# Optimization experiments

Measured on AMD Instinct MI355X. Metric: run time of the kernel, lower is better.

Reference implementation:

```python
import jax, jax.numpy as jnp
import numpy as np

L, D, H, N, R = 4, 256, 512, 16, 8  # layers, d_model, hidden=2*d_model, state_dim, dt_rank
OUT_LEN, IN_DIM = 96, 32
EPS = 1e-5


def _layernorm(v, g, b):
    m = jnp.mean(v, axis=-1, keepdims=True)
    var = jnp.mean((v - m) ** 2, axis=-1, keepdims=True)
    return (v - m) / jnp.sqrt(var + EPS) * g + b


def _pos_encoding(T, d):
    pos = jnp.arange(T, dtype=jnp.float32)[:, None]
    div = jnp.exp(jnp.arange(0, d, 2, dtype=jnp.float32) * (-np.log(10000.0) / d))
    pe = jnp.zeros((T, d), dtype=jnp.float32)
    pe = pe.at[:, 0::2].set(jnp.sin(pos * div))
    pe = pe.at[:, 1::2].set(jnp.cos(pos * div))
    return pe


def setup_inputs() -> dict:
    key = jax.random.key(0)
    ks = jax.random.split(key, 20)
    inp = {
        "x": jax.random.normal(ks[0], (8, 1024, IN_DIM), dtype=jnp.float32),
        "emb_w": jax.random.normal(ks[1], (D, IN_DIM), dtype=jnp.float32) * 0.1,
        "emb_b": jnp.zeros((D,), dtype=jnp.float32),
        "norm_g": jnp.ones((L, D), dtype=jnp.float32),
        "norm_b": jnp.zeros((L, D), dtype=jnp.float32),
        "in_w": jax.random.normal(ks[2], (L, H, D), dtype=jnp.float32) * (1.0 / np.sqrt(D)),
        "conv_w": jax.random.normal(ks[3], (L, H, 1, 3), dtype=jnp.float32) * 0.5,
        "A_p": jax.random.normal(ks[4], (L, H, N), dtype=jnp.float32) * 0.01,
        "D_p": jnp.ones((L, H), dtype=jnp.float32),
        "dt1_w": jax.random.normal(ks[5], (L, R, H), dtype=jnp.float32) * (1.0 / np.sqrt(H)),
        "dt1_b": jnp.zeros((L, R), dtype=jnp.float32),
        "dt2_w": jax.random.normal(ks[6], (L, H, R), dtype=jnp.float32) * (1.0 / np.sqrt(R)),
        "dt2_b": jnp.zeros((L, H), dtype=jnp.float32),
        "out_w": jax.random.normal(ks[7], (L, D, H), dtype=jnp.float32) * (1.0 / np.sqrt(H)),
        "final_g": jnp.ones((D,), dtype=jnp.float32),
        "final_b": jnp.zeros((D,), dtype=jnp.float32),
        "head1_w": jax.random.normal(ks[8], (D, D), dtype=jnp.float32) * (1.0 / np.sqrt(D)),
        "head1_b": jnp.zeros((D,), dtype=jnp.float32),
        "head2_w": jax.random.normal(ks[9], (OUT_LEN, D), dtype=jnp.float32) * (1.0 / np.sqrt(D)),
        "head2_b": jnp.zeros((OUT_LEN,), dtype=jnp.float32),
    }
    return inp


def _mamba_block(h, g, b, in_w, conv_w, A_p, D_p, dt1_w, dt1_b, dt2_w, dt2_b, out_w):
    res = h
    v = _layernorm(h, g, b)            # [B,T,D]
    v = jnp.einsum('btd,hd->bth', v, in_w)  # [B,T,H]
    # depthwise conv1d, kernel 3, padding 1, groups=H
    vc = jnp.transpose(v, (0, 2, 1))   # [B,H,T]
    vc = jax.lax.conv_general_dilated(vc, conv_w, window_strides=(1,),
                                      padding=[(1, 1)], feature_group_count=H,
                                      dimension_numbers=('NCH', 'OIH', 'NCH'))
    v = jnp.transpose(jax.nn.silu(vc), (0, 2, 1))  # [B,T,H]
    dt = jax.nn.relu(jnp.einsum('bth,rh->btr', v, dt1_w) + dt1_b)
    dt = jnp.einsum('btr,hr->bth', dt, dt2_w) + dt2_b
    dt = jax.nn.softplus(dt)           # [B,T,H]
    A = -jnp.exp(A_p)                  # [H,N]
    safe_A = jnp.where(jnp.abs(A) < 1e-5, jnp.ones_like(A), A)

    B_sz = v.shape[0]
    state0 = jnp.zeros((B_sz, H, N), dtype=v.dtype)

    def step(state, inp):
        x_t, dt_t = inp  # [B,H] each
        dA = A * dt_t[..., None]            # [B,H,N]
        discA = jnp.exp(dA)
        discB = (discA - 1.0) / safe_A * dt_t[..., None]
        state = discA * state + discB * x_t[..., None]
        y = jnp.einsum('bhn,hn->bh', state, A_p) + D_p * x_t
        return state, y

    xs = (jnp.transpose(v, (1, 0, 2)), jnp.transpose(dt, (1, 0, 2)))  # [T,B,H]
    _, ys = jax.lax.scan(step, state0, xs)
    y = jnp.transpose(ys, (1, 0, 2))   # [B,T,H]
    return res + jnp.einsum('bth,dh->btd', y, out_w)


def reference(x, emb_w, emb_b, norm_g, norm_b, in_w, conv_w, A_p, D_p,
              dt1_w, dt1_b, dt2_w, dt2_b, out_w, final_g, final_b,
              head1_w, head1_b, head2_w, head2_b):
    h = jnp.einsum('bti,di->btd', x, emb_w) + emb_b  # [B,T,D]
    h = h + _pos_encoding(h.shape[1], D)[None]
    for l in range(L):
        h = _mamba_block(h, norm_g[l], norm_b[l], in_w[l], conv_w[l], A_p[l],
                         D_p[l], dt1_w[l], dt1_b[l], dt2_w[l], dt2_b[l], out_w[l])
    h = _layernorm(h, final_g, final_b)
    h = h[:, -1, :]                    # last token [B,D]
    h = jax.nn.silu(h @ head1_w.T + head1_b)
    return h @ head2_w.T + head2_b     # [B, OUT_LEN]
```

## Files before the change

### kernel.cpp

```cpp
#include <hip/hip_runtime.h>
#include <hip/hip_bf16.h>
#include <math.h>

#define BB 8
#define TT 1024
#define DD 256
#define HH 512
#define NN 16
#define RR 8
#define OUT_LEN 96
#define IN_DIM 32
#define MM (BB*TT)

#define SC 16
#define CC (TT/SC)

typedef unsigned short u16;
typedef unsigned int u32;
typedef __attribute__((ext_vector_type(8))) short short8;
typedef __attribute__((ext_vector_type(8))) unsigned short u16x8;
typedef __attribute__((ext_vector_type(4))) float float4v;

__device__ __forceinline__ u16 f2bf(float f) {
    __hip_bfloat16 h = __float2bfloat16(f);
    return *(u16*)&h;
}
__device__ __forceinline__ float bf2f(u16 u) {
    u32 v = ((u32)u) << 16;
    return *(float*)&v;
}

#define GLD_LDS16(src, dst) __builtin_amdgcn_global_load_lds( \
    (const __attribute__((address_space(1))) void*)(src),     \
    (__attribute__((address_space(3))) void*)(dst), 16, 0, 0)

#define SBAR()   asm volatile("s_barrier" ::: "memory")
#define VMCNT0() asm volatile("s_waitcnt vmcnt(0)" ::: "memory")
#define VMCNT6() asm volatile("s_waitcnt vmcnt(6)" ::: "memory")
#define VMCNT9() asm volatile("s_waitcnt vmcnt(9)" ::: "memory")

__global__ __launch_bounds__(256) void embed_ln_cvt_kernel(
    const float* __restrict__ x, const float* __restrict__ emb_w,
    const float* __restrict__ emb_b,
    const float* __restrict__ g, const float* __restrict__ b,
    float* __restrict__ h, u16* __restrict__ lnout,
    const float* __restrict__ w_in, u16* __restrict__ wbf_in,
    const float* __restrict__ w_out, u16* __restrict__ wbf_out, int nw)
{
    int bid = blockIdx.x;
    if (bid >= MM) {
        int i = (bid - MM) * 256 + threadIdx.x;
        if (i < nw) wbf_in[i] = f2bf(w_in[i]);
        else        wbf_out[i - nw] = f2bf(w_out[i - nw]);
        return;
    }

    int bt = bid;
    int d  = threadIdx.x;
    int t  = bt & (TT - 1);

    __shared__ float xs[IN_DIM];
    __shared__ float red[4], red2[4];
    if (threadIdx.x < IN_DIM) xs[threadIdx.x] = x[bt * IN_DIM + threadIdx.x];
    __syncthreads();

    const float* w = emb_w + d * IN_DIM;
    float acc = emb_b[d];
#pragma unroll
    for (int i = 0; i < IN_DIM; i++) acc = fmaf(xs[i], w[i], acc);

    int i2 = d & ~1;
    float div = __expf(-(float)i2 * 0.0359778918f);
    float arg = (float)t * div;
    float pe = (d & 1) ? __cosf(arg) : __sinf(arg);
    float val = acc + pe;
    h[bt * DD + d] = val;

    float s = val;
#pragma unroll
    for (int o = 32; o > 0; o >>= 1) s += __shfl_down(s, o);
    int lane = d & 63, wave = d >> 6;
    if (lane == 0) red[wave] = s;
    __syncthreads();
    float mean = (red[0] + red[1] + red[2] + red[3]) * (1.0f / DD);

    float c = val - mean;
    float s2 = c * c;
#pragma unroll
    for (int o = 32; o > 0; o >>= 1) s2 += __shfl_down(s2, o);
    if (lane == 0) red2[wave] = s2;
    __syncthreads();
    float var = (red2[0] + red2[1] + red2[2] + red2[3]) * (1.0f / DD);

    lnout[bt * DD + d] = f2bf(c * rsqrtf(var + 1e-5f) * g[d] + b[d]);
}

template<int BM, int BN, int OUT_BF16>
__global__ __launch_bounds__(256) void gemm_bf16(
    const u16* __restrict__ A, const u16* __restrict__ B,
    void* __restrict__ Cv, int M, int N, int K, int addC)
{
    constexpr int BK = 64;
    constexpr int MT = BM / 32;
    constexpr int NT = BN / 32;
    static_assert(BM == 128 && BN == 64, "vmcnt count assumes 6 loads/thread");

    __shared__ __align__(16) u16 Al[2][8][BM][8];
    __shared__ __align__(16) u16 Bl[2][8][BN][8];

    const int tid = threadIdx.x;
    const int bm = blockIdx.y * BM;
    const int bn = blockIdx.x * BN;
    const int wid = tid >> 6, lane = tid & 63;
    const int wm = wid >> 1, wn = wid & 1;
    const int lq = lane >> 4, lm = lane & 15;

    float4v acc[MT][NT];
#pragma unroll
    for (int i = 0; i < MT; i++)
#pragma unroll
        for (int j = 0; j < NT; j++) acc[i][j] = (float4v){0.f, 0.f, 0.f, 0.f};

#pragma unroll
    for (int it = 0; it < (8 * BM) / 256; it++) {
        int c = it * 256 + tid;
        int q = c / BM, row = c % BM;
        GLD_LDS16(A + (size_t)(bm + row) * K + q * 8, &Al[0][q][row][0]);
    }
#pragma unroll
    for (int it = 0; it < (8 * BN) / 256; it++) {
        int c = it * 256 + tid;
        int q = c / BN, row = c % BN;
        GLD_LDS16(B + (size_t)(bn + row) * K + q * 8, &Bl[0][q][row][0]);
    }

    const int nt = K / BK;
    int cur = 0;
    for (int i = 0; i < nt; i++) {
        if (i + 1 < nt) {
            int nxt = cur ^ 1;
            int k1 = (i + 1) * BK;
#pragma unroll
            for (int it = 0; it < (8 * BM) / 256; it++) {
                int c = it * 256 + tid;
                int q = c / BM, row = c % BM;
                GLD_LDS16(A + (size_t)(bm + row) * K + k1 + q * 8, &Al[nxt][q][row][0]);
            }
#pragma unroll
            for (int it = 0; it < (8 * BN) / 256; it++) {
                int c = it * 256 + tid;
                int q = c / BN, row = c % BN;
                GLD_LDS16(B + (size_t)(bn + row) * K + k1 + q * 8, &Bl[nxt][q][row][0]);
            }
            VMCNT6();
        } else {
            VMCNT0();
        }
        SBAR();

        short8 af[2][MT], bf[2][NT];
#pragma unroll
        for (int kk = 0; kk < 2; kk++) {
#pragma unroll
            for (int mt = 0; mt < MT; mt++)
                af[kk][mt] = *(const short8*)&Al[cur][kk * 4 + lq][wm * (BM / 2) + mt * 16 + lm][0];
#pragma unroll
            for (int nt2 = 0; nt2 < NT; nt2++)
                bf[kk][nt2] = *(const short8*)&Bl[cur][kk * 4 + lq][wn * (BN / 2) + nt2 * 16 + lm][0];
        }

#pragma unroll
        for (int kk = 0; kk < 2; kk++)
#pragma unroll
            for (int mt = 0; mt < MT; mt++)
#pragma unroll
                for (int nt2 = 0; nt2 < NT; nt2++)
                    acc[mt][nt2] = __builtin_amdgcn_mfma_f32_16x16x32_bf16(
                        af[kk][mt], bf[kk][nt2], acc[mt][nt2], 0, 0, 0);
        SBAR();
        cur ^= 1;
    }

#pragma unroll
    for (int mt = 0; mt < MT; mt++)
#pragma unroll
        for (int nt2 = 0; nt2 < NT; nt2++) {
            int row0 = bm + wm * (BM / 2) + mt * 16 + lq * 4;
            int col  = bn + wn * (BN / 2) + nt2 * 16 + lm;
#pragma unroll
            for (int r = 0; r < 4; r++) {
                float vv = acc[mt][nt2][r];
                if (OUT_BF16) {
                    ((u16*)Cv)[(size_t)(row0 + r) * N + col] = f2bf(vv);
                } else {
                    float* cp = (float*)Cv + (size_t)(row0 + r) * N + col;
                    if (addC) vv += *cp;
                    *cp = vv;
                }
            }
        }
}

__global__ __launch_bounds__(256) void gemm2_ln(
    const u16* __restrict__ A, const u16* __restrict__ B,
    float* __restrict__ h,
    const float* __restrict__ g, const float* __restrict__ bb,
    u16* __restrict__ lnout, int doLN)
{
    constexpr int BM = 32;
    __shared__ __align__(16) u16 Al[2][8][BM][8];
    __shared__ __align__(16) u16 Bl[2][8][256][8];
    __shared__ float rs[2][BM], qs[2][BM];

    const int tid = threadIdx.x;
    const int bm = blockIdx.x * BM;
    const int wid = tid >> 6, lane = tid & 63;
    const int wm = wid >> 1, wn = wid & 1;
    const int lq = lane >> 4, lm = lane & 15;

    float4v acc[8];
#pragma unroll
    for (int j = 0; j < 8; j++) acc[j] = (float4v){0.f, 0.f, 0.f, 0.f};

    {
        int q = tid >> 5, row = tid & 31;
        GLD_LDS16(A + (size_t)(bm + row) * 512 + q * 8, &Al[0][q][row][0]);
    }
#pragma unroll
    for (int it = 0; it < 8; it++) {
        int c = it * 256 + tid;
        int q = c >> 8, row = c & 255;
        GLD_LDS16(B + (size_t)row * 512 + q * 8, &Bl[0][q][row][0]);
    }

    int cur = 0;
    for (int i = 0; i < 8; i++) {
        if (i + 1 < 8) {
            int nxt = cur ^ 1;
            int k1 = (i + 1) * 64;
            {
                int q = tid >> 5, row = tid & 31;
                GLD_LDS16(A + (size_t)(bm + row) * 512 + k1 + q * 8, &Al[nxt][q][row][0]);
            }
#pragma unroll
            for (int it = 0; it < 8; it++) {
                int c = it * 256 + tid;
                int q = c >> 8, row = c & 255;
                GLD_LDS16(B + (size_t)row * 512 + k1 + q * 8, &Bl[nxt][q][row][0]);
            }
            VMCNT9();
        } else {
            VMCNT0();
        }
        SBAR();

        short8 af[2], bf[2][8];
#pragma unroll
        for (int kk = 0; kk < 2; kk++) {
            af[kk] = *(const short8*)&Al[cur][kk * 4 + lq][wm * 16 + lm][0];
#pragma unroll
            for (int nt = 0; nt < 8; nt++)
                bf[kk][nt] = *(const short8*)&Bl[cur][kk * 4 + lq][wn * 128 + nt * 16 + lm][0];
        }
#pragma unroll
        for (int kk = 0; kk < 2; kk++)
#pragma unroll
            for (int nt = 0; nt < 8; nt++)
                acc[nt] = __builtin_amdgcn_mfma_f32_16x16x32_bf16(
                    af[kk], bf[kk][nt], acc[nt], 0, 0, 0);
        SBAR();
        cur ^= 1;
    }

    float val[4][8];
    float s1[4] = {0.f, 0.f, 0.f, 0.f}, s2[4] = {0.f, 0.f, 0.f, 0.f};
#pragma unroll
    for (int r = 0; r < 4; r++) {
        int row = bm + wm * 16 + lq * 4 + r;
#pragma unroll
        for (int nt = 0; nt < 8; nt++) {
            int col = wn * 128 + nt * 16 + lm;
            float v = acc[nt][r] + h[(size_t)row * DD + col];
            val[r][nt] = v;
            s1[r] += v;
            s2[r] = fmaf(v, v, s2[r]);
            h[(size_t)row * DD + col] = v;
        }
    }
#pragma unroll
    for (int r = 0; r < 4; r++) {
#pragma unroll
        for (int o = 1; o < 16; o <<= 1) {
            s1[r] += __shfl_xor(s1[r], o);
            s2[r] += __shfl_xor(s2[r], o);
        }
    }
    if (lm == 0) {
#pragma unroll
        for (int r = 0; r < 4; r++) {
            rs[wn][wm * 16 + lq * 4 + r] = s1[r];
            qs[wn][wm * 16 + lq * 4 + r] = s2[r];
        }
    }
    __syncthreads();

    if (doLN) {
#pragma unroll
        for (int r = 0; r < 4; r++) {
            int i = wm * 16 + lq * 4 + r;
            int row = bm + i;
            float mean = (rs[0][i] + rs[1][i]) * (1.0f / DD);
            float var  = (qs[0][i] + qs[1][i]) * (1.0f / DD) - mean * mean;
            float rstd = rsqrtf(var + 1e-5f);
#pragma unroll
            for (int nt = 0; nt < 8; nt++) {
                int col = wn * 128 + nt * 16 + lm;
                lnout[(size_t)row * DD + col] =
                    f2bf((val[r][nt] - mean) * rstd * g[col] + bb[col]);
            }
        }
    }
}

__device__ __forceinline__ float softplus_f(float s) {
    return (s > 20.0f) ? s : __logf(1.0f + __expf(s));
}

__global__ __launch_bounds__(512, 4) void conv_scan1(
    const u16* __restrict__ vbf, const float* __restrict__ cwg,
    const float* __restrict__ w1g, const float* __restrict__ b1g,
    const float* __restrict__ dt2_w, const float* __restrict__ dt2_b,
    const float* __restrict__ A_p,
    u16* __restrict__ vsb, float* __restrict__ dtr,
    u16* __restrict__ Lst, float* __restrict__ sdt)
{
    const int c = blockIdx.x;
    const int b = blockIdx.y;
    const int tid = threadIdx.x;
    const int wave = tid >> 6, lane = tid & 63;
    const int h0 = lane * 8;

    __shared__ float w1s[RR * 2 * 256];
    __shared__ u16   a_lds[SC][HH];
    __shared__ float ds[SC * RR];

#pragma unroll
    for (int i = 0; i < 2; i++) {
        int rci = wave + i * 8;
        int r = rci >> 1, jc = rci & 1;
        float4 wv = *(const float4*)(w1g + r * HH + lane * 8 + jc * 4);
        *(float4*)&w1s[rci * 256 + lane * 4] = wv;
    }
    __syncthreads();

    const float* wp = cwg + h0 * 3;
#pragma unroll
    for (int i = 0; i < 2; i++) {
        int tr = wave + i * 8;
        int t  = c * SC + tr;
        size_t m = (size_t)b * TT + t;

        const u16* vrow = vbf + m * HH + h0;
        u16x8 x0 = *(const u16x8*)vrow;
        u16x8 xm = (t > 0)      ? *(const u16x8*)(vrow - HH) : (u16x8)(0);
        u16x8 xp = (t < TT - 1) ? *(const u16x8*)(vrow + HH) : (u16x8)(0);

        float a[8];
        u16x8 o;
#pragma unroll
        for (int j = 0; j < 8; j++) {
            float s = wp[j * 3] * bf2f(xm[j]);
            s = fmaf(wp[j * 3 + 1], bf2f(x0[j]), s);
            s = fmaf(wp[j * 3 + 2], bf2f(xp[j]), s);
            s = s / (1.0f + __expf(-s));
            a[j] = s;
            o[j] = f2bf(s);
        }
        *(u16x8*)(vsb + m * HH + h0) = o;
        *(u16x8*)&a_lds[tr][h0]      = o;

        float acc[RR];
#pragma unroll
        for (int r = 0; r < RR; r++) {
            float4 wlo = *(const float4*)&w1s[(r * 2 + 0) * 256 + lane * 4];
            float4 whi = *(const float4*)&w1s[(r * 2 + 1) * 256 + lane * 4];
            float s = a[0] * wlo.x;
            s = fmaf(a[1], wlo.y, s);
            s = fmaf(a[2], wlo.z, s);
            s = fmaf(a[3], wlo.w, s);
            s = fmaf(a[4], whi.x, s);
            s = fmaf(a[5], whi.y, s);
            s = fmaf(a[6], whi.z, s);
            s = fmaf(a[7], whi.w, s);
            acc[r] = s;
        }
#pragma unroll
        for (int r = 0; r < RR; r++) {
#pragma unroll
            for (int o2 = 1; o2 < 64; o2 <<= 1) acc[r] += __shfl_xor(acc[r], o2);
        }
        if (lane == 0) {
#pragma unroll
            for (int r = 0; r < RR; r++) acc[r] = fmaxf(acc[r] + b1g[r], 0.0f);
            *(float4*)(dtr + m * RR)     = make_float4(acc[0], acc[1], acc[2], acc[3]);
            *(float4*)(dtr + m * RR + 4) = make_float4(acc[4], acc[5], acc[6], acc[7]);
#pragma unroll
            for (int r = 0; r < RR; r++) ds[tr * RR + r] = acc[r];
        }
    }
    __syncthreads();

    const int h = tid;
    float A2[NN], invA[NN], st[NN];
    const float* ap = A_p + h * NN;
#pragma unroll
    for (int n = 0; n < NN; n++) {
        float av = -__expf(ap[n]);
        A2[n] = av * 1.44269504f;
        invA[n] = 1.0f / av;
        st[n] = 0.0f;
    }
    float w2[RR];
#pragma unroll
    for (int r = 0; r < RR; r++) w2[r] = dt2_w[h * RR + r];
    float b2 = dt2_b[h];

    float xv = bf2f(a_lds[0][h]);
    float s_dt = 0.0f;
#pragma unroll 2
    for (int t = 0; t < SC; t++) {
        float xn = (t + 1 < SC) ? bf2f(a_lds[t + 1][h]) : 0.0f;
        float s = b2;
#pragma unroll
        for (int r = 0; r < RR; r++) s = fmaf(ds[t * RR + r], w2[r], s);
        float dt = softplus_f(s);
        s_dt += dt;
        float dtx = dt * xv;
#pragma unroll
        for (int n = 0; n < NN; n++) {
            float e = __builtin_amdgcn_exp2f(A2[n] * dt);
            float u = invA[n] * dtx;
            st[n] = fmaf(e, st[n] + u, -u);
        }
        xv = xn;
    }

    size_t base = (((size_t)c * BB + b) * HH + h) * NN;
    u16x8 lo, hi;
#pragma unroll
    for (int n = 0; n < 8; n++) { lo[n] = f2bf(st[n]); hi[n] = f2bf(st[n + 8]); }
    *(u16x8*)(Lst + base)     = lo;
    *(u16x8*)(Lst + base + 8) = hi;
    sdt[((size_t)c * BB + b) * HH + h] = s_dt;
}

__global__ __launch_bounds__(256) void scan_carry_par(
    const float* __restrict__ A_p, const float* __restrict__ sdt,
    u16* __restrict__ Lst)
{
    int gw   = (blockIdx.x << 2) | (threadIdx.x >> 6);
    int lane = threadIdx.x & 63;
    int b = gw >> 9;
    int h = gw & 511;

    size_t sidx = ((size_t)lane * BB + b) * HH + h;
    float sd = sdt[sidx];
    const float* ap = A_p + h * NN;
    u16x8 Llo = *(const u16x8*)(Lst + sidx * NN);
    u16x8 Lhi = *(const u16x8*)(Lst + sidx * NN + 8);
    u16x8 Elo, Ehi;
#pragma unroll
    for (int n = 0; n < NN; n++) {
        float An = -__expf(ap[n]);
        float p  = __expf(An * sd);
        float lv = bf2f((n < 8) ? Llo[n] : Lhi[n - 8]);
#pragma unroll
        for (int d2 = 1; d2 < 64; d2 <<= 1) {
            float pp = __shfl_up(p, d2);
            float pl = __shfl_up(lv, d2);
            if (lane >= d2) { lv = fmaf(pl, p, lv); p = pp * p; }
        }
        float E = __shfl_up(lv, 1);
        if (lane == 0) E = 0.0f;
        if (n < 8) Elo[n] = f2bf(E); else Ehi[n - 8] = f2bf(E);
    }
    *(u16x8*)(Lst + sidx * NN)     = Elo;
    *(u16x8*)(Lst + sidx * NN + 8) = Ehi;
}

__global__ __launch_bounds__(256, 4) void scan_pass2(
    const u16* __restrict__ vs,
    const float* __restrict__ dtr,
    const float* __restrict__ dt2_w,
    const float* __restrict__ dt2_b,
    const float* __restrict__ A_p, const float* __restrict__ D_p,
    const u16* __restrict__ carry,
    u16* __restrict__ y)
{
    int h = blockIdx.x * 256 + threadIdx.x;
    int c = blockIdx.y;
    int b = blockIdx.z;

    __shared__ float ds[SC * RR];
    {
        const float* drow = dtr + ((size_t)b * TT + (size_t)c * SC) * RR;
        if (threadIdx.x < SC * RR) ds[threadIdx.x] = drow[threadIdx.x];
    }

    float A2[NN], invA[NN], Ap[NN], st[NN];
    const float* app = A_p + h * NN;
    size_t cbase = (((size_t)c * BB + b) * HH + h) * NN;
    {
        u16x8 lo = *(const u16x8*)(carry + cbase);
        u16x8 hi = *(const u16x8*)(carry + cbase + 8);
#pragma unroll
        for (int n = 0; n < 8; n++) { st[n] = bf2f(lo[n]); st[n + 8] = bf2f(hi[n]); }
    }
#pragma unroll
    for (int n = 0; n < NN; n++) {
        float apv = app[n];
        Ap[n] = apv;
        float a = -__expf(apv);
        A2[n] = a * 1.44269504f;
        invA[n] = 1.0f / a;
    }
    float w2[RR];
#pragma unroll
    for (int r = 0; r < RR; r++) w2[r] = dt2_w[h * RR + r];
    float b2 = dt2_b[h];
    float Dp = D_p[h];

    const u16* vbase = vs + ((size_t)b * TT + (size_t)c * SC) * HH + h;
    u16*       ybase = y  + ((size_t)b * TT + (size_t)c * SC) * HH + h;
    float xv = bf2f(vbase[0]);
    __syncthreads();

#pragma unroll 2
    for (int t = 0; t < SC; t++) {
        float xn = (t + 1 < SC) ? bf2f(vbase[(size_t)(t + 1) * HH]) : 0.0f;
        float s = b2;
#pragma unroll
        for (int r = 0; r < RR; r++) s = fmaf(ds[t * RR + r], w2[r], s);
        float dt = softplus_f(s);
        float dtx = dt * xv;
        float acc = Dp * xv;
#pragma unroll
        for (int n = 0; n < NN; n++) {
            float e = __builtin_amdgcn_exp2f(A2[n] * dt);
            float u = invA[n] * dtx;
            st[n] = fmaf(e, st[n] + u, -u);
            acc = fmaf(st[n], Ap[n], acc);
        }
        ybase[(size_t)t * HH] = f2bf(acc);
        xv = xn;
    }
}

__global__ __launch_bounds__(256) void head_kernel(
    const float* __restrict__ h,
    const float* __restrict__ fg, const float* __restrict__ fb,
    const float* __restrict__ w1, const float* __restrict__ b1,
    const float* __restrict__ w2, const float* __restrict__ b2,
    float* __restrict__ out)
{
    int b = blockIdx.x;
    int d = threadIdx.x;
    __shared__ float hn[DD], s1[DD];
    __shared__ float red[4];

    float v = h[((size_t)b * TT + (TT - 1)) * DD + d];

    float s = v;
#pragma unroll
    for (int o = 32; o > 0; o >>= 1) s += __shfl_down(s, o);
    int lane = d & 63, wave = d >> 6;
    if (lane == 0) red[wave] = s;
    __syncthreads();
    float mean = (red[0] + red[1] + red[2] + red[3]) * (1.0f / DD);
    __syncthreads();

    float c = v - mean;
    float s2 = c * c;
#pragma unroll
    for (int o = 32; o > 0; o >>= 1) s2 += __shfl_down(s2, o);
    if (lane == 0) red[wave] = s2;
    __syncthreads();
    float var = (red[0] + red[1] + red[2] + red[3]) * (1.0f / DD);

    hn[d] = c * rsqrtf(var + 1e-5f) * fg[d] + fb[d];
    __syncthreads();

    float a1 = b1[d];
    const float* w1r = w1 + d * DD;
#pragma unroll 8
    for (int k = 0; k < DD; k++) a1 = fmaf(hn[k], w1r[k], a1);
    s1[d] = a1 / (1.0f + __expf(-a1));
    __syncthreads();

    if (d < OUT_LEN) {
        float a2 = b2[d];
        const float* w2r = w2 + d * DD;
#pragma unroll 8
        for (int k = 0; k < DD; k++) a2 = fmaf(s1[k], w2r[k], a2);
        out[b * OUT_LEN + d] = a2;
    }
}

extern "C" void kernel_launch(void* const* d_in, const int* in_sizes, int n_in,
                              void* d_out, int out_size, void* d_ws, size_t ws_size,
                              hipStream_t stream)
{
    (void)in_sizes; (void)n_in; (void)out_size; (void)ws_size;

    const float* x       = (const float*)d_in[0];
    const float* emb_w   = (const float*)d_in[1];
    const float* emb_b   = (const float*)d_in[2];
    const float* norm_g  = (const float*)d_in[3];
    const float* norm_b  = (const float*)d_in[4];
    const float* in_w    = (const float*)d_in[5];
    const float* conv_w  = (const float*)d_in[6];
    const float* A_p     = (const float*)d_in[7];
    const float* D_p     = (const float*)d_in[8];
    const float* dt1_w   = (const float*)d_in[9];
    const float* dt1_b   = (const float*)d_in[10];
    const float* dt2_w   = (const float*)d_in[11];
    const float* dt2_b   = (const float*)d_in[12];
    const float* out_w   = (const float*)d_in[13];
    const float* final_g = (const float*)d_in[14];
    const float* final_b = (const float*)d_in[15];
    const float* head1_w = (const float*)d_in[16];
    const float* head1_b = (const float*)d_in[17];
    const float* head2_w = (const float*)d_in[18];
    const float* head2_b = (const float*)d_in[19];
    float* outp = (float*)d_out;

    char* ws = (char*)d_ws;
    float* h     = (float*)ws;                ws += (size_t)MM * DD * 4;
    u16*   vbf   = (u16*)ws;                  ws += (size_t)MM * HH * 2;
    u16*   vsb   = (u16*)ws;                  ws += (size_t)MM * HH * 2;
    u16*   ybf   = (u16*)ws;                  ws += (size_t)MM * HH * 2;
    u16*   lnbuf = (u16*)ws;                  ws += (size_t)MM * DD * 2;
    float* dtr   = (float*)ws;                ws += (size_t)MM * RR * 4;
    u16*   Lst   = (u16*)ws;                  ws += (size_t)CC * BB * HH * NN * 2;
    float* sdt   = (float*)ws;                ws += (size_t)CC * BB * HH * 4;
    u16*   wbf_in  = (u16*)ws;                ws += (size_t)4 * HH * DD * 2;
    u16*   wbf_out = (u16*)ws;                ws += (size_t)4 * DD * HH * 2;

    const int NW = 4 * HH * DD;
    embed_ln_cvt_kernel<<<MM + (2 * NW) / 256, 256, 0, stream>>>(
        x, emb_w, emb_b, norm_g, norm_b, h, lnbuf,
        in_w, wbf_in, out_w, wbf_out, NW);

    for (int l = 0; l < 4; l++) {
        gemm_bf16<128, 64, 1><<<dim3(HH / 64, MM / 128), 256, 0, stream>>>(
            lnbuf, wbf_in + (size_t)l * HH * DD, vbf, MM, HH, DD, 0);

        conv_scan1<<<dim3(CC, BB), 512, 0, stream>>>(
            vbf, conv_w + (size_t)l * HH * 3,
            dt1_w + (size_t)l * RR * HH, dt1_b + l * RR,
            dt2_w + (size_t)l * HH * RR, dt2_b + l * HH,
            A_p + (size_t)l * HH * NN,
            vsb, dtr, Lst, sdt);

        scan_carry_par<<<(BB * HH) / 4, 256, 0, stream>>>(
            A_p + (size_t)l * HH * NN, sdt, Lst);

        scan_pass2<<<dim3(HH / 256, CC, BB), 256, 0, stream>>>(
            vsb, dtr, dt2_w + (size_t)l * HH * RR, dt2_b + l * HH,
            A_p + (size_t)l * HH * NN, D_p + l * HH, Lst, ybf);

        const float* g_next = (l < 3) ? (norm_g + (l + 1) * DD) : final_g;
        const float* b_next = (l < 3) ? (norm_b + (l + 1) * DD) : final_b;
        gemm2_ln<<<MM / 32, 256, 0, stream>>>(
            ybf, wbf_out + (size_t)l * DD * HH, h, g_next, b_next,
            lnbuf, (l < 3) ? 1 : 0);
    }

    head_kernel<<<BB, 256, 0, stream>>>(h, final_g, final_b,
                                        head1_w, head1_b, head2_w, head2_b, outp);
}
```

Baseline: 485.7 us.

## Fuse scan pass2 into out-projection GEMM with LayerNorm epilogue

Merges the second scan pass and the out-projection GEMM+LayerNorm into one kernel. Each 512-thread block scans 32 timesteps (two chunks) for all 512 hidden channels, writes y into an XOR-swizzled LDS tile, and then runs the MFMA GEMM against the out_w tile straight from LDS. This removes the bf16 y buffer round trip through global memory and one kernel launch per layer. In exchange there are fewer blocks in flight (large LDS, 512 threads), each thread runs a serial scan over 32 steps, and the GEMM N-split across waves becomes finer.

```diff
diff --git a/kernel.cpp b/kernel.cpp
--- a/kernel.cpp
+++ b/kernel.cpp
@@ -36,8 +36,8 @@
 
 #define SBAR()   asm volatile("s_barrier" ::: "memory")
 #define VMCNT0() asm volatile("s_waitcnt vmcnt(0)" ::: "memory")
+#define VMCNT4() asm volatile("s_waitcnt vmcnt(4)" ::: "memory")
 #define VMCNT6() asm volatile("s_waitcnt vmcnt(6)" ::: "memory")
-#define VMCNT9() asm volatile("s_waitcnt vmcnt(9)" ::: "memory")
 
 __global__ __launch_bounds__(256) void embed_ln_cvt_kernel(
     const float* __restrict__ x, const float* __restrict__ emb_w,
@@ -201,127 +201,6 @@
         }
 }
 
-__global__ __launch_bounds__(256) void gemm2_ln(
-    const u16* __restrict__ A, const u16* __restrict__ B,
-    float* __restrict__ h,
-    const float* __restrict__ g, const float* __restrict__ bb,
-    u16* __restrict__ lnout, int doLN)
-{
-    constexpr int BM = 32;
-    __shared__ __align__(16) u16 Al[2][8][BM][8];
-    __shared__ __align__(16) u16 Bl[2][8][256][8];
-    __shared__ float rs[2][BM], qs[2][BM];
-
-    const int tid = threadIdx.x;
-    const int bm = blockIdx.x * BM;
-    const int wid = tid >> 6, lane = tid & 63;
-    const int wm = wid >> 1, wn = wid & 1;
-    const int lq = lane >> 4, lm = lane & 15;
-
-    float4v acc[8];
-#pragma unroll
-    for (int j = 0; j < 8; j++) acc[j] = (float4v){0.f, 0.f, 0.f, 0.f};
-
-    {
-        int q = tid >> 5, row = tid & 31;
-        GLD_LDS16(A + (size_t)(bm + row) * 512 + q * 8, &Al[0][q][row][0]);
-    }
-#pragma unroll
-    for (int it = 0; it < 8; it++) {
-        int c = it * 256 + tid;
-        int q = c >> 8, row = c & 255;
-        GLD_LDS16(B + (size_t)row * 512 + q * 8, &Bl[0][q][row][0]);
-    }
-
-    int cur = 0;
-    for (int i = 0; i < 8; i++) {
-        if (i + 1 < 8) {
-            int nxt = cur ^ 1;
-            int k1 = (i + 1) * 64;
-            {
-                int q = tid >> 5, row = tid & 31;
-                GLD_LDS16(A + (size_t)(bm + row) * 512 + k1 + q * 8, &Al[nxt][q][row][0]);
-            }
-#pragma unroll
-            for (int it = 0; it < 8; it++) {
-                int c = it * 256 + tid;
-                int q = c >> 8, row = c & 255;
-                GLD_LDS16(B + (size_t)row * 512 + k1 + q * 8, &Bl[nxt][q][row][0]);
-            }
-            VMCNT9();
-        } else {
-            VMCNT0();
-        }
-        SBAR();
-
-        short8 af[2], bf[2][8];
-#pragma unroll
-        for (int kk = 0; kk < 2; kk++) {
-            af[kk] = *(const short8*)&Al[cur][kk * 4 + lq][wm * 16 + lm][0];
-#pragma unroll
-            for (int nt = 0; nt < 8; nt++)
-                bf[kk][nt] = *(const short8*)&Bl[cur][kk * 4 + lq][wn * 128 + nt * 16 + lm][0];
-        }
-#pragma unroll
-        for (int kk = 0; kk < 2; kk++)
-#pragma unroll
-            for (int nt = 0; nt < 8; nt++)
-                acc[nt] = __builtin_amdgcn_mfma_f32_16x16x32_bf16(
-                    af[kk], bf[kk][nt], acc[nt], 0, 0, 0);
-        SBAR();
-        cur ^= 1;
-    }
-
-    float val[4][8];
-    float s1[4] = {0.f, 0.f, 0.f, 0.f}, s2[4] = {0.f, 0.f, 0.f, 0.f};
-#pragma unroll
-    for (int r = 0; r < 4; r++) {
-        int row = bm + wm * 16 + lq * 4 + r;
-#pragma unroll
-        for (int nt = 0; nt < 8; nt++) {
-            int col = wn * 128 + nt * 16 + lm;
-            float v = acc[nt][r] + h[(size_t)row * DD + col];
-            val[r][nt] = v;
-            s1[r] += v;
-            s2[r] = fmaf(v, v, s2[r]);
-            h[(size_t)row * DD + col] = v;
-        }
-    }
-#pragma unroll
-    for (int r = 0; r < 4; r++) {
-#pragma unroll
-        for (int o = 1; o < 16; o <<= 1) {
-            s1[r] += __shfl_xor(s1[r], o);
-            s2[r] += __shfl_xor(s2[r], o);
-        }
-    }
-    if (lm == 0) {
-#pragma unroll
-        for (int r = 0; r < 4; r++) {
-            rs[wn][wm * 16 + lq * 4 + r] = s1[r];
-            qs[wn][wm * 16 + lq * 4 + r] = s2[r];
-        }
-    }
-    __syncthreads();
-
-    if (doLN) {
-#pragma unroll
-        for (int r = 0; r < 4; r++) {
-            int i = wm * 16 + lq * 4 + r;
-            int row = bm + i;
-            float mean = (rs[0][i] + rs[1][i]) * (1.0f / DD);
-            float var  = (qs[0][i] + qs[1][i]) * (1.0f / DD) - mean * mean;
-            float rstd = rsqrtf(var + 1e-5f);
-#pragma unroll
-            for (int nt = 0; nt < 8; nt++) {
-                int col = wn * 128 + nt * 16 + lm;
-                lnout[(size_t)row * DD + col] =
-                    f2bf((val[r][nt] - mean) * rstd * g[col] + bb[col]);
-            }
-        }
-    }
-}
-
 __device__ __forceinline__ float softplus_f(float s) {
     return (s > 20.0f) ? s : __logf(1.0f + __expf(s));
 }
@@ -488,71 +367,186 @@
     *(u16x8*)(Lst + sidx * NN + 8) = Ehi;
 }
 
-__global__ __launch_bounds__(256, 4) void scan_pass2(
-    const u16* __restrict__ vs,
-    const float* __restrict__ dtr,
-    const float* __restrict__ dt2_w,
-    const float* __restrict__ dt2_b,
+__global__ __launch_bounds__(512) void scan2_gemm2_ln(
+    const u16* __restrict__ vsb, const float* __restrict__ dtr,
+    const float* __restrict__ dt2_w, const float* __restrict__ dt2_b,
     const float* __restrict__ A_p, const float* __restrict__ D_p,
     const u16* __restrict__ carry,
-    u16* __restrict__ y)
+    const u16* __restrict__ B,
+    float* __restrict__ h,
+    const float* __restrict__ g, const float* __restrict__ bb,
+    u16* __restrict__ lnout, int doLN)
 {
-    int h = blockIdx.x * 256 + threadIdx.x;
-    int c = blockIdx.y;
-    int b = blockIdx.z;
-
-    __shared__ float ds[SC * RR];
-    {
-        const float* drow = dtr + ((size_t)b * TT + (size_t)c * SC) * RR;
-        if (threadIdx.x < SC * RR) ds[threadIdx.x] = drow[threadIdx.x];
-    }
-
-    float A2[NN], invA[NN], Ap[NN], st[NN];
-    const float* app = A_p + h * NN;
-    size_t cbase = (((size_t)c * BB + b) * HH + h) * NN;
-    {
-        u16x8 lo = *(const u16x8*)(carry + cbase);
-        u16x8 hi = *(const u16x8*)(carry + cbase + 8);
-#pragma unroll
-        for (int n = 0; n < 8; n++) { st[n] = bf2f(lo[n]); st[n + 8] = bf2f(hi[n]); }
-    }
+    const int bid = blockIdx.x;
+    const int b   = bid >> 5;
+    const int tb  = bid & 31;
+    const int t0  = tb * 32;
+    const int c0  = tb * 2;
+    const int bm  = bid * 32;
+
+    const int tid = threadIdx.x;
+    const int wid = tid >> 6;
+    const int lane = tid & 63;
+    const int lq = lane >> 4, lm = lane & 15;
+    const int wm = wid >> 2;
+    const int wn = wid & 3;
+
+    __shared__ __align__(16) u16 Yl[32 * 512];
+    __shared__ __align__(16) u16 Bl[2][8][256][8];
+    __shared__ float ds[32 * RR];
+    __shared__ float rs[4][32], qs[4][32];
+
+#pragma unroll
+    for (int it = 0; it < 4; it++) {
+        int cth = it * 512 + tid;
+        int q = cth >> 8, row = cth & 255;
+        GLD_LDS16(B + (size_t)row * 512 + q * 8, &Bl[0][q][row][0]);
+    }
+
+    if (tid < 256) {
+        int tr = tid >> 3, r = tid & 7;
+        ds[tid] = dtr[((size_t)b * TT + t0 + tr) * RR + r];
+    }
+
+    const int hh = tid;
+    float A2[NN], invA[NN], Ap[NN], w2[RR];
+    const float* ap = A_p + hh * NN;
 #pragma unroll
     for (int n = 0; n < NN; n++) {
-        float apv = app[n];
-        Ap[n] = apv;
+        float apv = ap[n]; Ap[n] = apv;
         float a = -__expf(apv);
-        A2[n] = a * 1.44269504f;
-        invA[n] = 1.0f / a;
-    }
-    float w2[RR];
-#pragma unroll
-    for (int r = 0; r < RR; r++) w2[r] = dt2_w[h * RR + r];
-    float b2 = dt2_b[h];
-    float Dp = D_p[h];
-
-    const u16* vbase = vs + ((size_t)b * TT + (size_t)c * SC) * HH + h;
-    u16*       ybase = y  + ((size_t)b * TT + (size_t)c * SC) * HH + h;
-    float xv = bf2f(vbase[0]);
-    __syncthreads();
-
+        A2[n] = a * 1.44269504f; invA[n] = 1.0f / a;
+    }
+#pragma unroll
+    for (int r = 0; r < RR; r++) w2[r] = dt2_w[hh * RR + r];
+    float b2 = dt2_b[hh];
+    float Dp = D_p[hh];
+    __syncthreads();
+
+#pragma unroll
+    for (int cc = 0; cc < 2; cc++) {
+        int cg = c0 + cc;
+        float st[NN];
+        size_t cbase = (((size_t)cg * BB + b) * HH + hh) * NN;
+        u16x8 clo = *(const u16x8*)(carry + cbase);
+        u16x8 chi = *(const u16x8*)(carry + cbase + 8);
+#pragma unroll
+        for (int n = 0; n < 8; n++) { st[n] = bf2f(clo[n]); st[n + 8] = bf2f(chi[n]); }
+
+        const u16* vbase = vsb + ((size_t)b * TT + (size_t)cg * SC) * HH + hh;
+        float xv = bf2f(vbase[0]);
 #pragma unroll 2
-    for (int t = 0; t < SC; t++) {
-        float xn = (t + 1 < SC) ? bf2f(vbase[(size_t)(t + 1) * HH]) : 0.0f;
-        float s = b2;
-#pragma unroll
-        for (int r = 0; r < RR; r++) s = fmaf(ds[t * RR + r], w2[r], s);
-        float dt = softplus_f(s);
-        float dtx = dt * xv;
-        float acc = Dp * xv;
-#pragma unroll
-        for (int n = 0; n < NN; n++) {
-            float e = __builtin_amdgcn_exp2f(A2[n] * dt);
-            float u = invA[n] * dtx;
-            st[n] = fmaf(e, st[n] + u, -u);
-            acc = fmaf(st[n], Ap[n], acc);
-        }
-        ybase[(size_t)t * HH] = f2bf(acc);
-        xv = xn;
+        for (int t = 0; t < SC; t++) {
+            float xn = (t + 1 < SC) ? bf2f(vbase[(size_t)(t + 1) * HH]) : 0.0f;
+            int tr = cc * SC + t;
+            float s = b2;
+#pragma unroll
+            for (int r = 0; r < RR; r++) s = fmaf(ds[tr * RR + r], w2[r], s);
+            float dt = softplus_f(s);
+            float dtx = dt * xv;
+            float acc = Dp * xv;
+#pragma unroll
+            for (int n = 0; n < NN; n++) {
+                float e = __builtin_amdgcn_exp2f(A2[n] * dt);
+                float u = invA[n] * dtx;
+                st[n] = fmaf(e, st[n] + u, -u);
+                acc = fmaf(st[n], Ap[n], acc);
+            }
+            Yl[tr * 512 + (hh ^ ((tr & 7) << 3))] = f2bf(acc);
+            xv = xn;
+        }
+    }
+    __syncthreads();
+
+    float4v acc4[4];
+#pragma unroll
+    for (int j = 0; j < 4; j++) acc4[j] = (float4v){0.f, 0.f, 0.f, 0.f};
+
+    int cur = 0;
+    for (int i = 0; i < 8; i++) {
+        if (i + 1 < 8) {
+            int nxt = cur ^ 1;
+            int k1 = (i + 1) * 64;
+#pragma unroll
+            for (int it = 0; it < 4; it++) {
+                int cth = it * 512 + tid;
+                int q = cth >> 8, row = cth & 255;
+                GLD_LDS16(B + (size_t)row * 512 + k1 + q * 8, &Bl[nxt][q][row][0]);
+            }
+            VMCNT4();
+        } else {
+            VMCNT0();
+        }
+        SBAR();
+
+        int k0 = i * 64;
+        short8 af[2], bf[2][4];
+#pragma unroll
+        for (int kk = 0; kk < 2; kk++) {
+            int row = wm * 16 + lm;
+            int kg  = (k0 >> 3) + kk * 4 + lq;
+            af[kk] = *(const short8*)&Yl[row * 512 + ((kg ^ (row & 7)) << 3)];
+#pragma unroll
+            for (int nt = 0; nt < 4; nt++)
+                bf[kk][nt] = *(const short8*)&Bl[cur][kk * 4 + lq][wn * 64 + nt * 16 + lm][0];
+        }
+#pragma unroll
+        for (int kk = 0; kk < 2; kk++)
+#pragma unroll
+            for (int nt = 0; nt < 4; nt++)
+                acc4[nt] = __builtin_amdgcn_mfma_f32_16x16x32_bf16(
+                    af[kk], bf[kk][nt], acc4[nt], 0, 0, 0);
+        SBAR();
+        cur ^= 1;
+    }
+
+    float val[4][4];
+    float s1[4] = {0.f, 0.f, 0.f, 0.f}, s2[4] = {0.f, 0.f, 0.f, 0.f};
+#pragma unroll
+    for (int r = 0; r < 4; r++) {
+        int row = bm + wm * 16 + lq * 4 + r;
+#pragma unroll
+        for (int nt = 0; nt < 4; nt++) {
+            int col = wn * 64 + nt * 16 + lm;
+            float v = acc4[nt][r] + h[(size_t)row * DD + col];
+            val[r][nt] = v;
+            s1[r] += v;
+            s2[r] = fmaf(v, v, s2[r]);
+            h[(size_t)row * DD + col] = v;
+        }
+    }
+#pragma unroll
+    for (int r = 0; r < 4; r++) {
+#pragma unroll
+        for (int o = 1; o < 16; o <<= 1) {
+            s1[r] += __shfl_xor(s1[r], o);
+            s2[r] += __shfl_xor(s2[r], o);
+        }
+    }
+    if (lm == 0) {
+#pragma unroll
+        for (int r = 0; r < 4; r++) {
+            rs[wn][wm * 16 + lq * 4 + r] = s1[r];
+            qs[wn][wm * 16 + lq * 4 + r] = s2[r];
+        }
+    }
+    __syncthreads();
+
+    if (doLN) {
+#pragma unroll
+        for (int r = 0; r < 4; r++) {
+            int i = wm * 16 + lq * 4 + r;
+            int row = bm + i;
+            float mean = (rs[0][i] + rs[1][i] + rs[2][i] + rs[3][i]) * (1.0f / DD);
+            float var  = (qs[0][i] + qs[1][i] + qs[2][i] + qs[3][i]) * (1.0f / DD) - mean * mean;
+            float rstd = rsqrtf(var + 1e-5f);
+#pragma unroll
+            for (int nt = 0; nt < 4; nt++) {
+                int col = wn * 64 + nt * 16 + lm;
+                lnout[(size_t)row * DD + col] =
+                    f2bf((val[r][nt] - mean) * rstd * g[col] + bb[col]);
+            }
+        }
     }
 }
 
@@ -638,7 +632,6 @@
     float* h     = (float*)ws;                ws += (size_t)MM * DD * 4;
     u16*   vbf   = (u16*)ws;                  ws += (size_t)MM * HH * 2;
     u16*   vsb   = (u16*)ws;                  ws += (size_t)MM * HH * 2;
-    u16*   ybf   = (u16*)ws;                  ws += (size_t)MM * HH * 2;
     u16*   lnbuf = (u16*)ws;                  ws += (size_t)MM * DD * 2;
     float* dtr   = (float*)ws;                ws += (size_t)MM * RR * 4;
     u16*   Lst   = (u16*)ws;                  ws += (size_t)CC * BB * HH * NN * 2;
@@ -665,15 +658,13 @@
         scan_carry_par<<<(BB * HH) / 4, 256, 0, stream>>>(
             A_p + (size_t)l * HH * NN, sdt, Lst);
 
-        scan_pass2<<<dim3(HH / 256, CC, BB), 256, 0, stream>>>(
-            vsb, dtr, dt2_w + (size_t)l * HH * RR, dt2_b + l * HH,
-            A_p + (size_t)l * HH * NN, D_p + l * HH, Lst, ybf);
-
         const float* g_next = (l < 3) ? (norm_g + (l + 1) * DD) : final_g;
         const float* b_next = (l < 3) ? (norm_b + (l + 1) * DD) : final_b;
-        gemm2_ln<<<MM / 32, 256, 0, stream>>>(
-            ybf, wbf_out + (size_t)l * DD * HH, h, g_next, b_next,
-            lnbuf, (l < 3) ? 1 : 0);
+        scan2_gemm2_ln<<<MM / 32, 512, 0, stream>>>(
+            vsb, dtr, dt2_w + (size_t)l * HH * RR, dt2_b + l * HH,
+            A_p + (size_t)l * HH * NN, D_p + l * HH,
+            Lst, wbf_out + (size_t)l * DD * HH,
+            h, g_next, b_next, lnbuf, (l < 3) ? 1 : 0);
     }
 
     head_kernel<<<BB, 256, 0, stream>>>(h, final_g, final_b,
```

After: 468.1 us. 1.04x faster.
